# Kernel tuning notes

Measured on AMD Instinct MI355X. Metric: run time of the kernel, lower is better.

## Reference

```python
import jax, jax.numpy as jnp
import numpy as np

N_NODES = 100000
N_EDGES = 1600000
F_IN = 128
F_OUT = 128


def _spmm(edge_row, edge_col, edge_weight, X):
    # sparse [N,N] @ dense [N,F]: gather source rows, weight, scatter-add to dest rows
    msgs = edge_weight[:, None] * X[edge_col]  # [E, F]
    return jax.ops.segment_sum(msgs, edge_row, num_segments=N_NODES)


def setup_inputs() -> dict:
    key = jax.random.key(0)
    ks = jax.random.split(key, 7)
    scale = 1.0 / np.sqrt(F_IN)
    return {
        "x": jax.random.normal(ks[0], (N_NODES, F_IN), dtype=jnp.float32),
        "edge_row": jax.random.randint(ks[1], (N_EDGES,), 0, N_NODES, dtype=jnp.int32),
        "edge_col": jax.random.randint(ks[2], (N_EDGES,), 0, N_NODES, dtype=jnp.int32),
        "edge_weight": jax.random.uniform(ks[3], (N_EDGES,), dtype=jnp.float32),
        "w1": jax.random.normal(ks[4], (F_IN, F_IN), dtype=jnp.float32) * scale,
        "w2": jax.random.normal(ks[5], (F_IN, F_OUT), dtype=jnp.float32) * scale,
        "w3": jax.random.normal(ks[6], (F_OUT, F_OUT), dtype=jnp.float32) * scale,
    }


def reference(x, edge_row, edge_col, edge_weight, w1, w2, w3):
    # dropout p=0.0 (eval) -> identity
    h = jax.nn.relu(_spmm(edge_row, edge_col, edge_weight, x @ w1))
    h = jax.nn.relu(_spmm(edge_row, edge_col, edge_weight, h @ w2))
    h = jax.nn.relu(_spmm(edge_row, edge_col, edge_weight, h @ w3))
    return h
```

## Files before the change

### kernel.cpp

```cpp
#include <hip/hip_runtime.h>

#define N_NODES 100000
#define N_EDGES 1600000
#define F 128

#define SCAN_B 1024
#define SCAN_NB ((N_NODES + SCAN_B - 1) / SCAN_B)

#define NSHARD 8
#define SHARD_RANGE ((N_NODES + NSHARD - 1) / NSHARD)

typedef short bf16x8 __attribute__((ext_vector_type(8)));
typedef float f32x4  __attribute__((ext_vector_type(4)));

union ABFrag {
    bf16x8 v;
    unsigned short u[8];
    uint4  q;
};

__device__ __forceinline__ unsigned short f2bf(float f) {
    unsigned int u = __float_as_uint(f);
    u += 0x7fffu + ((u >> 16) & 1u);
    return (unsigned short)(u >> 16);
}
__device__ __forceinline__ float bflo(unsigned int u) {
    return __uint_as_float(u << 16);
}
__device__ __forceinline__ float bfhi(unsigned int u) {
    return __uint_as_float(u & 0xFFFF0000u);
}


__global__ __launch_bounds__(256) void edge_prep(
    const int* __restrict__ erow, const int* __restrict__ ecol,
    const float* __restrict__ ew,
    int* __restrict__ counts, unsigned long long* __restrict__ rec) {
    const int e = blockIdx.x * blockDim.x + threadIdx.x;
    const int dst = erow[e];
    const unsigned int r = (unsigned int)atomicAdd(&counts[dst], 1);
    const unsigned int colw = ((unsigned int)ecol[e] << 15) | (unsigned int)f2bf(ew[e]);
    rec[e] = ((unsigned long long)(((unsigned int)dst << 8) | (r & 255u)) << 32) | colw;
}

__global__ void scan_block_sums(const int* __restrict__ counts, int* __restrict__ bsums) {
    __shared__ int s[SCAN_B];
    const int t = threadIdx.x;
    const int idx = blockIdx.x * SCAN_B + t;
    int v = (idx < N_NODES) ? counts[idx] : 0;
    s[t] = v;
    __syncthreads();
    for (int off = SCAN_B / 2; off > 0; off >>= 1) {
        if (t < off) s[t] += s[t + off];
        __syncthreads();
    }
    if (t == 0) bsums[blockIdx.x] = s[0];
}

__global__ void scan_bsums(const int* __restrict__ bsums, int* __restrict__ boffs) {
    __shared__ int s[128];
    const int t = threadIdx.x;
    int v = (t < SCAN_NB) ? bsums[t] : 0;
    s[t] = v;
    __syncthreads();
    for (int off = 1; off < 128; off <<= 1) {
        int u = (t >= off) ? s[t - off] : 0;
        __syncthreads();
        s[t] += u;
        __syncthreads();
    }
    if (t < SCAN_NB) boffs[t] = s[t] - v;
}

__global__ void scan_final(const int* __restrict__ counts, const int* __restrict__ boffs,
                           int* __restrict__ row_ptr) {
    __shared__ int s[SCAN_B];
    const int t = threadIdx.x;
    const int idx = blockIdx.x * SCAN_B + t;
    int v = (idx < N_NODES) ? counts[idx] : 0;
    s[t] = v;
    __syncthreads();
    for (int off = 1; off < SCAN_B; off <<= 1) {
        int u = (t >= off) ? s[t - off] : 0;
        __syncthreads();
        s[t] += u;
        __syncthreads();
    }
    if (idx < N_NODES) row_ptr[idx] = boffs[blockIdx.x] + s[t] - v;
    if (idx == 0) row_ptr[N_NODES] = N_EDGES;
}

__global__ __launch_bounds__(256) void csr_fill_sharded(
    const unsigned long long* __restrict__ rec,
    const int* __restrict__ row_ptr,
    unsigned int* __restrict__ pairs) {
    const int shard = blockIdx.x & (NSHARD - 1);
    const int e = (blockIdx.x >> 3) * 256 + threadIdx.x;
    const unsigned long long v = rec[e];
    const unsigned int hi = (unsigned int)(v >> 32);
    const int dst = (int)(hi >> 8);
    const unsigned int lo = (unsigned int)(shard * SHARD_RANGE);
    if ((unsigned int)(dst - lo) < (unsigned int)SHARD_RANGE) {
        const int rank = (int)(hi & 255u);
        pairs[row_ptr[dst] + rank] = (unsigned int)v;
    }
}

__global__ void transpose_w_bf16(const float* __restrict__ W, unsigned short* __restrict__ Wt) {
    const int i = blockIdx.x * 256 + threadIdx.x;
    const int n = i >> 7;
    const int k = i & 127;
    Wt[i] = f2bf(W[k * F + n]);
}

__global__ __launch_bounds__(256) void gemm_mfma(
    const float* __restrict__ Xf,
    const unsigned short* __restrict__ Xb,
    const unsigned short* __restrict__ Wt,
    unsigned short* __restrict__ Y,
    int use_f32_in)
{
    __shared__ unsigned short Wl[4 * 8 * 64 * 8];

    const int tid  = threadIdx.x;
    const int wave = tid >> 6;
    const int lane = tid & 63;

    for (int s = tid; s < 2048; s += 256) {
        const int ln  = s & 63;
        const int ntk = s >> 6;
        const int nt  = ntk & 7;
        const int kt  = ntk >> 3;
        const int n   = nt * 16 + (ln & 15);
        const int k   = kt * 32 + (ln >> 4) * 8;
        *(uint4*)(&Wl[s * 8]) = *(const uint4*)(Wt + n * F + k);
    }
    __syncthreads();

    const int m     = blockIdx.x * 64 + wave * 16 + (lane & 15);
    const bool mval = (m < N_NODES);
    const int kq    = (lane >> 4) * 8;

    f32x4 acc[8] = {};

#pragma unroll
    for (int kt = 0; kt < 4; ++kt) {
        ABFrag a;
        if (mval) {
            if (use_f32_in) {
                const float* p = Xf + (size_t)m * F + kt * 32 + kq;
                const float4 u0 = *(const float4*)p;
                const float4 u1 = *(const float4*)(p + 4);
                a.u[0] = f2bf(u0.x); a.u[1] = f2bf(u0.y);
                a.u[2] = f2bf(u0.z); a.u[3] = f2bf(u0.w);
                a.u[4] = f2bf(u1.x); a.u[5] = f2bf(u1.y);
                a.u[6] = f2bf(u1.z); a.u[7] = f2bf(u1.w);
            } else {
                a.q = *(const uint4*)(Xb + (size_t)m * F + kt * 32 + kq);
#pragma unroll
                for (int j = 0; j < 8; ++j)
                    if (a.u[j] & 0x8000u) a.u[j] = 0;
            }
        } else {
            a.q = make_uint4(0, 0, 0, 0);
        }
#pragma unroll
        for (int nt = 0; nt < 8; ++nt) {
            ABFrag b;
            b.q = *(const uint4*)(&Wl[((kt * 8 + nt) * 64 + lane) * 8]);
            acc[nt] = __builtin_amdgcn_mfma_f32_16x16x32_bf16(a.v, b.v, acc[nt], 0, 0, 0);
        }
    }

    const int rbase = blockIdx.x * 64 + wave * 16 + (lane >> 4) * 4;
    const int cbase = lane & 15;
#pragma unroll
    for (int r = 0; r < 4; ++r) {
        const int row = rbase + r;
        if (row < N_NODES) {
#pragma unroll
            for (int nt = 0; nt < 8; ++nt) {
                Y[(size_t)row * F + nt * 16 + cbase] = f2bf(acc[nt][r]);
            }
        }
    }
}

__global__ __launch_bounds__(256) void spmm_csr_bf16(
    const unsigned short* __restrict__ Xb,
    const int* __restrict__ row_ptr,
    const unsigned int* __restrict__ pairs,
    unsigned short* __restrict__ Ob,
    float* __restrict__ Of,
    int final_mode) {
    const int tid = threadIdx.x;
    const int l16 = tid & 15;
    const int q   = tid >> 4;
    const int row = blockIdx.x * 16 + q;

    const int beg = row_ptr[row];
    const int end = row_ptr[row + 1];

    float a[8] = {};
    int i = beg;
    for (; i + 1 < end; i += 2) {
        const unsigned int p0 = pairs[i], p1 = pairs[i + 1];
        const uint4 v0 = *(const uint4*)(Xb + (size_t)(p0 >> 15) * F + l16 * 8);
        const uint4 v1 = *(const uint4*)(Xb + (size_t)(p1 >> 15) * F + l16 * 8);
        const float w0 = bflo(p0 & 0x7FFFu);
        const float w1 = bflo(p1 & 0x7FFFu);
        a[0] += w0 * bflo(v0.x); a[1] += w0 * bfhi(v0.x);
        a[2] += w0 * bflo(v0.y); a[3] += w0 * bfhi(v0.y);
        a[4] += w0 * bflo(v0.z); a[5] += w0 * bfhi(v0.z);
        a[6] += w0 * bflo(v0.w); a[7] += w0 * bfhi(v0.w);
        a[0] += w1 * bflo(v1.x); a[1] += w1 * bfhi(v1.x);
        a[2] += w1 * bflo(v1.y); a[3] += w1 * bfhi(v1.y);
        a[4] += w1 * bflo(v1.z); a[5] += w1 * bfhi(v1.z);
        a[6] += w1 * bflo(v1.w); a[7] += w1 * bfhi(v1.w);
    }
    if (i < end) {
        const unsigned int p0 = pairs[i];
        const uint4 v0 = *(const uint4*)(Xb + (size_t)(p0 >> 15) * F + l16 * 8);
        const float w0 = bflo(p0 & 0x7FFFu);
        a[0] += w0 * bflo(v0.x); a[1] += w0 * bfhi(v0.x);
        a[2] += w0 * bflo(v0.y); a[3] += w0 * bfhi(v0.y);
        a[4] += w0 * bflo(v0.z); a[5] += w0 * bfhi(v0.z);
        a[6] += w0 * bflo(v0.w); a[7] += w0 * bfhi(v0.w);
    }

    if (final_mode) {
        float4 o0 = {fmaxf(a[0], 0.f), fmaxf(a[1], 0.f), fmaxf(a[2], 0.f), fmaxf(a[3], 0.f)};
        float4 o1 = {fmaxf(a[4], 0.f), fmaxf(a[5], 0.f), fmaxf(a[6], 0.f), fmaxf(a[7], 0.f)};
        float* p = Of + (size_t)row * F + l16 * 8;
        *(float4*)p = o0;
        *(float4*)(p + 4) = o1;
    } else {
        uint4 o;
        o.x = (unsigned int)f2bf(a[0]) | ((unsigned int)f2bf(a[1]) << 16);
        o.y = (unsigned int)f2bf(a[2]) | ((unsigned int)f2bf(a[3]) << 16);
        o.z = (unsigned int)f2bf(a[4]) | ((unsigned int)f2bf(a[5]) << 16);
        o.w = (unsigned int)f2bf(a[6]) | ((unsigned int)f2bf(a[7]) << 16);
        *(uint4*)(Ob + (size_t)row * F + l16 * 8) = o;
    }
}


extern "C" void kernel_launch(void* const* d_in, const int* in_sizes, int n_in,
                              void* d_out, int out_size, void* d_ws, size_t ws_size,
                              hipStream_t stream) {
    const float* x    = (const float*)d_in[0];
    const int*   erow = (const int*)d_in[1];
    const int*   ecol = (const int*)d_in[2];
    const float* ew   = (const float*)d_in[3];
    const float* w1   = (const float*)d_in[4];
    const float* w2   = (const float*)d_in[5];
    const float* w3   = (const float*)d_in[6];
    float* out = (float*)d_out;

    char* ws = (char*)d_ws;
    size_t off = 0;
    auto alloc = [&](size_t bytes) -> char* {
        char* p = ws + off;
        off += (bytes + 255) & ~(size_t)255;
        return p;
    };
    unsigned short* bufA = (unsigned short*)alloc((size_t)N_NODES * F * 2);
    unsigned short* bufB = (unsigned short*)alloc((size_t)N_NODES * F * 2);
    unsigned int* pairs  = (unsigned int*)alloc((size_t)N_EDGES * 4);
    int* counts  = (int*)alloc((size_t)N_NODES * sizeof(int));
    int* row_ptr = (int*)alloc(((size_t)N_NODES + 1) * sizeof(int));
    int* bsums   = (int*)alloc((size_t)SCAN_NB * sizeof(int));
    int* boffs   = (int*)alloc((size_t)SCAN_NB * sizeof(int));
    unsigned short* wt1 = (unsigned short*)alloc((size_t)F * F * 2);
    unsigned short* wt2 = (unsigned short*)alloc((size_t)F * F * 2);
    unsigned short* wt3 = (unsigned short*)alloc((size_t)F * F * 2);

    unsigned long long* rec = (unsigned long long*)bufB;

    hipMemsetAsync(counts, 0, (size_t)N_NODES * sizeof(int), stream);
    edge_prep<<<N_EDGES / 256, 256, 0, stream>>>(erow, ecol, ew, counts, rec);
    scan_block_sums<<<SCAN_NB, SCAN_B, 0, stream>>>(counts, bsums);
    scan_bsums<<<1, 128, 0, stream>>>(bsums, boffs);
    scan_final<<<SCAN_NB, SCAN_B, 0, stream>>>(counts, boffs, row_ptr);
    csr_fill_sharded<<<(N_EDGES / 256) * NSHARD, 256, 0, stream>>>(rec, row_ptr, pairs);

    transpose_w_bf16<<<64, 256, 0, stream>>>(w1, wt1);
    transpose_w_bf16<<<64, 256, 0, stream>>>(w2, wt2);
    transpose_w_bf16<<<64, 256, 0, stream>>>(w3, wt3);

    const int ggrid = (N_NODES + 63) / 64;
    const int sgrid = N_NODES / 16;

    gemm_mfma<<<ggrid, 256, 0, stream>>>(x, nullptr, wt1, bufA, 1);
    spmm_csr_bf16<<<sgrid, 256, 0, stream>>>(bufA, row_ptr, pairs, bufB, nullptr, 0);
    gemm_mfma<<<ggrid, 256, 0, stream>>>(nullptr, bufB, wt2, bufA, 0);
    spmm_csr_bf16<<<sgrid, 256, 0, stream>>>(bufA, row_ptr, pairs, bufB, nullptr, 0);
    gemm_mfma<<<ggrid, 256, 0, stream>>>(nullptr, bufB, wt3, bufA, 0);
    spmm_csr_bf16<<<sgrid, 256, 0, stream>>>(bufA, row_ptr, pairs, nullptr, out, 1);
}
```

Before: 447.6 us.

## Replace global-atomic CSR build with chunked LDS histograms and deterministic ranks

Edge binning no longer uses global atomics on per-node counters. Each of 128 chunks builds packed 8-bit per-node histograms in LDS, done in two halves of the node range. A per-node prefix over chunks gives base offsets, and a second pass computes each edge's final CSR position, so the fill kernel only checks a position range per shard and scatters. This trades contended global atomics for extra passes over edge_row, per-chunk count arrays in global memory, and only 128 blocks per pass. The packed 8-bit counters assume small per-node degrees.

```diff
diff --git a/kernel.cpp b/kernel.cpp
--- a/kernel.cpp
+++ b/kernel.cpp
@@ -8,7 +8,11 @@
 #define SCAN_NB ((N_NODES + SCAN_B - 1) / SCAN_B)
 
 #define NSHARD 8
-#define SHARD_RANGE ((N_NODES + NSHARD - 1) / NSHARD)
+#define SHARD_E (N_EDGES / NSHARD)
+
+#define NCHUNK 128
+#define CHUNK_E (N_EDGES / NCHUNK)
+#define HALF_N 50000
 
 typedef short bf16x8 __attribute__((ext_vector_type(8)));
 typedef float f32x4  __attribute__((ext_vector_type(4)));
@@ -32,15 +36,42 @@
 }
 
 
-__global__ __launch_bounds__(256) void edge_prep(
-    const int* __restrict__ erow, const int* __restrict__ ecol,
-    const float* __restrict__ ew,
-    int* __restrict__ counts, unsigned long long* __restrict__ rec) {
-    const int e = blockIdx.x * blockDim.x + threadIdx.x;
-    const int dst = erow[e];
-    const unsigned int r = (unsigned int)atomicAdd(&counts[dst], 1);
-    const unsigned int colw = ((unsigned int)ecol[e] << 15) | (unsigned int)f2bf(ew[e]);
-    rec[e] = ((unsigned long long)(((unsigned int)dst << 8) | (r & 255u)) << 32) | colw;
+__global__ __launch_bounds__(256) void chunk_hist(
+    const int* __restrict__ erow, unsigned char* __restrict__ counts8) {
+    __shared__ unsigned int h[HALF_N / 4];
+    const int c = blockIdx.x;
+    const int t = threadIdx.x;
+#pragma unroll
+    for (int half = 0; half < 2; ++half) {
+        for (int i = t; i < HALF_N / 4; i += 256) h[i] = 0;
+        __syncthreads();
+        const int lo = half * HALF_N;
+        for (int e = c * CHUNK_E + t; e < (c + 1) * CHUNK_E; e += 256) {
+            const unsigned int d = (unsigned int)(erow[e] - lo);
+            if (d < HALF_N) atomicAdd(&h[d >> 2], 1u << ((d & 3u) * 8u));
+        }
+        __syncthreads();
+        unsigned int* dw = (unsigned int*)(counts8 + (size_t)c * N_NODES + lo);
+        for (int i = t; i < HALF_N / 4; i += 256) dw[i] = h[i];
+        __syncthreads();
+    }
+}
+
+__global__ __launch_bounds__(256) void chunk_prefix(
+    const unsigned char* __restrict__ counts8,
+    unsigned char* __restrict__ base8, int* __restrict__ counts) {
+    const int w = blockIdx.x * 256 + threadIdx.x;
+    if (w >= N_NODES / 4) return;
+    unsigned int run = 0;
+    for (int c = 0; c < NCHUNK; ++c) {
+        ((unsigned int*)(base8 + (size_t)c * N_NODES))[w] = run;
+        run += ((const unsigned int*)(counts8 + (size_t)c * N_NODES))[w];
+    }
+    const int n = w * 4;
+    counts[n + 0] = run & 255u;
+    counts[n + 1] = (run >> 8) & 255u;
+    counts[n + 2] = (run >> 16) & 255u;
+    counts[n + 3] = run >> 24;
 }
 
 __global__ void scan_block_sums(const int* __restrict__ counts, int* __restrict__ bsums) {
@@ -90,19 +121,46 @@
     if (idx == 0) row_ptr[N_NODES] = N_EDGES;
 }
 
+__global__ __launch_bounds__(256) void chunk_rank(
+    const int* __restrict__ erow, const int* __restrict__ ecol,
+    const float* __restrict__ ew,
+    const unsigned char* __restrict__ base8, const int* __restrict__ row_ptr,
+    unsigned long long* __restrict__ rec) {
+    __shared__ unsigned int h[HALF_N / 4];
+    const int c = blockIdx.x;
+    const int t = threadIdx.x;
+#pragma unroll
+    for (int half = 0; half < 2; ++half) {
+        for (int i = t; i < HALF_N / 4; i += 256) h[i] = 0;
+        __syncthreads();
+        const int lo = half * HALF_N;
+        for (int e = c * CHUNK_E + t; e < (c + 1) * CHUNK_E; e += 256) {
+            const int dst = erow[e];
+            const unsigned int d = (unsigned int)(dst - lo);
+            if (d < HALF_N) {
+                const unsigned int old = atomicAdd(&h[d >> 2], 1u << ((d & 3u) * 8u));
+                const unsigned int lrank = (old >> ((d & 3u) * 8u)) & 255u;
+                const unsigned int pos = (unsigned int)row_ptr[dst]
+                                       + (unsigned int)base8[(size_t)c * N_NODES + dst]
+                                       + lrank;
+                const unsigned int colw = ((unsigned int)ecol[e] << 15)
+                                        | (unsigned int)f2bf(ew[e]);
+                rec[e] = ((unsigned long long)pos << 32) | colw;
+            }
+        }
+        __syncthreads();
+    }
+}
+
 __global__ __launch_bounds__(256) void csr_fill_sharded(
     const unsigned long long* __restrict__ rec,
-    const int* __restrict__ row_ptr,
     unsigned int* __restrict__ pairs) {
     const int shard = blockIdx.x & (NSHARD - 1);
     const int e = (blockIdx.x >> 3) * 256 + threadIdx.x;
     const unsigned long long v = rec[e];
-    const unsigned int hi = (unsigned int)(v >> 32);
-    const int dst = (int)(hi >> 8);
-    const unsigned int lo = (unsigned int)(shard * SHARD_RANGE);
-    if ((unsigned int)(dst - lo) < (unsigned int)SHARD_RANGE) {
-        const int rank = (int)(hi & 255u);
-        pairs[row_ptr[dst] + rank] = (unsigned int)v;
+    const unsigned int pos = (unsigned int)(v >> 32);
+    if ((unsigned int)(pos - (unsigned int)(shard * SHARD_E)) < (unsigned int)SHARD_E) {
+        pairs[pos] = (unsigned int)v;
     }
 }
 
@@ -275,14 +333,17 @@
     unsigned short* wt2 = (unsigned short*)alloc((size_t)F * F * 2);
     unsigned short* wt3 = (unsigned short*)alloc((size_t)F * F * 2);
 
+    unsigned char* counts8 = (unsigned char*)bufA;
+    unsigned char* base8   = (unsigned char*)bufA + (size_t)NCHUNK * N_NODES;
     unsigned long long* rec = (unsigned long long*)bufB;
 
-    hipMemsetAsync(counts, 0, (size_t)N_NODES * sizeof(int), stream);
-    edge_prep<<<N_EDGES / 256, 256, 0, stream>>>(erow, ecol, ew, counts, rec);
+    chunk_hist<<<NCHUNK, 256, 0, stream>>>(erow, counts8);
+    chunk_prefix<<<(N_NODES / 4 + 255) / 256, 256, 0, stream>>>(counts8, base8, counts);
     scan_block_sums<<<SCAN_NB, SCAN_B, 0, stream>>>(counts, bsums);
     scan_bsums<<<1, 128, 0, stream>>>(bsums, boffs);
     scan_final<<<SCAN_NB, SCAN_B, 0, stream>>>(counts, boffs, row_ptr);
-    csr_fill_sharded<<<(N_EDGES / 256) * NSHARD, 256, 0, stream>>>(rec, row_ptr, pairs);
+    chunk_rank<<<NCHUNK, 256, 0, stream>>>(erow, ecol, ew, base8, row_ptr, rec);
+    csr_fill_sharded<<<(N_EDGES / 256) * NSHARD, 256, 0, stream>>>(rec, pairs);
 
     transpose_w_bf16<<<64, 256, 0, stream>>>(w1, wt1);
     transpose_w_bf16<<<64, 256, 0, stream>>>(w2, wt2);
```

After: 494.9 us. 10.6% more time.
